# Kernel tuning notes

Hardware: AMD Instinct MI355X
Metric: run time of the kernel (lower is better)

The kernel has to match this reference:

```python
import jax, jax.numpy as jnp
import numpy as np
from jax import lax

NUM_GROUP = 512
GROUP_SIZE = 32


def fps(xyz, npoint):
    """Farthest point sampling. xyz: [B, N, 3] -> centers [B, npoint, 3]."""
    B, N, _ = xyz.shape
    big = jnp.asarray(1e10, xyz.dtype)

    def body(carry, _):
        min_d, farthest = carry  # [B, N], [B]
        centroid = jnp.take_along_axis(xyz, farthest[:, None, None], axis=1)  # [B,1,3]
        d = jnp.sum((xyz - centroid) ** 2, axis=-1)  # [B, N]
        min_d = jnp.minimum(min_d, d)
        nxt = jnp.argmax(min_d, axis=-1).astype(jnp.int32)
        return (min_d, nxt), farthest

    init = (jnp.full((B, N), big, xyz.dtype), jnp.zeros((B,), jnp.int32))
    _, idxs = lax.scan(body, init, None, length=npoint)  # [npoint, B]
    idxs = idxs.T  # [B, npoint]
    return jnp.take_along_axis(xyz, idxs[..., None], axis=1)  # [B, npoint, 3]


def knn_idx(xyz, center, k):
    """xyz [B,N,3], center [B,G,3] -> idx [B,G,k] of k nearest (squared L2)."""
    # [B, G, N] squared distances
    d2 = jnp.sum((center[:, :, None, :] - xyz[:, None, :, :]) ** 2, axis=-1)
    _, idx = lax.top_k(-d2, k)  # smallest distances
    return idx


def setup_inputs() -> dict:
    key = jax.random.key(0)
    xyz = jax.random.normal(key, (32, 3, 8192), dtype=jnp.float32)
    return {"xyz": xyz}


def reference(xyz):
    # xyz: [B, 3, N] -> [B, N, 3]
    pts = jnp.transpose(xyz, (0, 2, 1))[:, :, :3]
    B, N, _ = pts.shape
    center = fps(pts, NUM_GROUP)                  # [B, G, 3]
    idx = knn_idx(pts, center, GROUP_SIZE)        # [B, G, k]
    flat_idx = idx.reshape(B, NUM_GROUP * GROUP_SIZE)
    neighborhood = jnp.take_along_axis(pts, flat_idx[..., None], axis=1)
    neighborhood = neighborhood.reshape(B, NUM_GROUP, GROUP_SIZE, 3)
    neighborhood = neighborhood - center[:, :, None, :]
    return neighborhood, center
```

## Files before the change

### kernel.cpp

```cpp
#include <hip/hip_runtime.h>

typedef unsigned long long u64;
typedef unsigned int u32;
typedef float v2f __attribute__((ext_vector_type(2)));

#define BATCH 32
#define NPTS  8192
#define NGRP  512
#define KNN_K 32

#define FPS_T 256
#define FPS_W (FPS_T / 64)
#define PPAIR (NPTS / FPS_T / 2)

#define KNN_WPB 8
#define KNN_T   (KNN_WPB * 64)
#define QCAP    128

#define NCH     (NPTS / 64)
#define GC      16
#define NCELL   (GC * GC * GC)
#define QB      512
#define BT      512
#define BPT     (NPTS / BT)
#define WSF     (4 * NPTS + NCH * 6)

__device__ __forceinline__ float sq3(float dx, float dy, float dz) {
    return __fadd_rn(__fadd_rn(__fmul_rn(dx, dx), __fmul_rn(dy, dy)), __fmul_rn(dz, dz));
}

__device__ __forceinline__ u64 packdi(float d, int n) {
    return ((u64)__float_as_uint(d) << 32) | (u32)n;
}

__device__ __forceinline__ u64 umin64(u64 a, u64 b) { return a < b ? a : b; }
__device__ __forceinline__ u64 umax64(u64 a, u64 b) { return a > b ? a : b; }

__device__ __forceinline__ u64 shfl_xor_u64(u64 v, int m) {
    int lo = __shfl_xor((int)(u32)v, m, 64);
    int hi = __shfl_xor((int)(u32)(v >> 32), m, 64);
    return ((u64)(u32)hi << 32) | (u32)lo;
}

__device__ __forceinline__ u64 shfl_u64(u64 v, int src) {
    int lo = __shfl((int)(u32)v, src, 64);
    int hi = __shfl((int)(u32)(v >> 32), src, 64);
    return ((u64)(u32)hi << 32) | (u32)lo;
}

template <int CTRL>
__device__ __forceinline__ u64 dpp_max_step(u64 k) {
    u32 plo = (u32)__builtin_amdgcn_update_dpp(0, (int)(u32)k, CTRL, 0xF, 0xF, true);
    u32 phi = (u32)__builtin_amdgcn_update_dpp(0, (int)(u32)(k >> 32), CTRL, 0xF, 0xF, true);
    u64 p = ((u64)phi << 32) | plo;
    return k > p ? k : p;
}
__device__ __forceinline__ u64 dpp_wave_max(u64 k) {
    k = dpp_max_step<0x111>(k);
    k = dpp_max_step<0x112>(k);
    k = dpp_max_step<0x114>(k);
    k = dpp_max_step<0x118>(k);
    k = dpp_max_step<0x142>(k);
    k = dpp_max_step<0x143>(k);
    return k;
}

__device__ __forceinline__ u64 lane_sort64(u64 v, int lane) {
#pragma unroll
    for (int k = 2; k <= 64; k <<= 1) {
#pragma unroll
        for (int j = k >> 1; j > 0; j >>= 1) {
            u64 p = shfl_xor_u64(v, j);
            bool keepmin = (((lane & k) == 0) == ((lane & j) == 0));
            u64 mn = umin64(v, p), mx = umax64(v, p);
            v = keepmin ? mn : mx;
        }
    }
    return v;
}

__device__ __forceinline__ u64 lane_merge64(u64 m, u64 c, int lane) {
    u64 cr = shfl_xor_u64(c, 63);
    u64 z = umin64(m, cr);
#pragma unroll
    for (int dd = 32; dd > 0; dd >>= 1) {
        u64 p = shfl_xor_u64(z, dd);
        u64 mn = umin64(z, p), mx = umax64(z, p);
        z = (lane & dd) ? mx : mn;
    }
    return z;
}

__device__ __forceinline__ void knn_step(u64& m, u64& tau, int& cnt, u64* sbuf,
                                         float x, float y, float z,
                                         float cx, float cy, float cz,
                                         int n, int lane) {
    float d = sq3(__fsub_rn(x, cx), __fsub_rn(y, cy), __fsub_rn(z, cz));
    u64 kk = packdi(d, n);
    bool cand = kk < tau;
    u64 mask = __ballot(cand);
    if (mask) {
        u32 below = __builtin_amdgcn_mbcnt_hi(
            (u32)(mask >> 32), __builtin_amdgcn_mbcnt_lo((u32)mask, 0));
        if (cand) sbuf[cnt + below] = kk;
        cnt += (int)__popcll(mask);
        if (cnt >= 64) {
            u64 c = sbuf[lane];
            c = lane_sort64(c, lane);
            m = lane_merge64(m, c, lane);
            tau = shfl_u64(m, 31);
            int rem = cnt - 64;
            if (lane < rem) sbuf[lane] = sbuf[64 + lane];
            cnt = rem;
        }
    }
}

__global__ __launch_bounds__(FPS_T) void fps_kernel(const float* __restrict__ in,
                                                    float* __restrict__ centers) {
#pragma clang fp contract(off)
    __shared__ float sx[NPTS];
    __shared__ float sy[NPTS];
    __shared__ float sz[NPTS];
    __shared__ u64 s_key[2][FPS_W];
    __shared__ float s_out[NGRP * 3];

    const int b = blockIdx.x;
    const int t = threadIdx.x;
    const int w = t >> 6;
    const float* xp = in + (size_t)b * 3 * NPTS;
    const float* yp = xp + NPTS;
    const float* zp = xp + 2 * NPTS;

    v2f xr[PPAIR], yr[PPAIR], zr[PPAIR], md[PPAIR];
#pragma unroll
    for (int i = 0; i < PPAIR; ++i) {
        int n = i * (2 * FPS_T) + 2 * t;
        xr[i] = *(const v2f*)(xp + n);
        yr[i] = *(const v2f*)(yp + n);
        zr[i] = *(const v2f*)(zp + n);
        *(v2f*)(sx + n) = xr[i];
        *(v2f*)(sy + n) = yr[i];
        *(v2f*)(sz + n) = zr[i];
        md[i] = (v2f){1e10f, 1e10f};
    }
    __syncthreads();

    int cur = 0;
    for (int r = 0; r < NGRP; ++r) {
        const float cx = sx[cur], cy = sy[cur], cz = sz[cur];
        if (t == 0) {
            s_out[r * 3 + 0] = cx;
            s_out[r * 3 + 1] = cy;
            s_out[r * 3 + 2] = cz;
        }

        float bd0 = -1.0f, bd1 = -1.0f;
        int   bi0 = 0,     bi1 = 0;
#pragma unroll
        for (int i = 0; i < PPAIR; ++i) {
            v2f dx = xr[i] - cx;
            v2f dy = yr[i] - cy;
            v2f dz = zr[i] - cz;
            v2f dd = dx * dx + dy * dy + dz * dz;
            md[i] = __builtin_elementwise_min(md[i], dd);
            int n = i * (2 * FPS_T) + 2 * t;
            if (md[i].x > bd0) { bd0 = md[i].x; bi0 = n; }
            if (md[i].y > bd1) { bd1 = md[i].y; bi1 = n + 1; }
        }
        u64 k0 = ((u64)__float_as_uint(bd0) << 32) | (u32)(~(u32)bi0);
        u64 k1 = ((u64)__float_as_uint(bd1) << 32) | (u32)(~(u32)bi1);
        u64 k = dpp_wave_max(umax64(k0, k1));
        if ((t & 63) == 63) s_key[r & 1][w] = k;
        __syncthreads();
        u64 m = umax64(umax64(s_key[r & 1][0], s_key[r & 1][1]),
                       umax64(s_key[r & 1][2], s_key[r & 1][3]));
        cur = (int)(~(u32)m);
    }

    __syncthreads();
    float* cdst = centers + (size_t)b * NGRP * 3;
    for (int i = t; i < NGRP * 3; i += FPS_T) cdst[i] = s_out[i];
}

__device__ __forceinline__ int qbin(float v) {
    int c = (int)((v + 4.0f) * 64.0f);
    c = c < 0 ? 0 : c;
    return c > (QB - 1) ? (QB - 1) : c;
}
__device__ __forceinline__ u32 part3_4(u32 v) {
    return (v & 1u) | ((v & 2u) << 2) | ((v & 4u) << 4) | ((v & 8u) << 6);
}

__global__ __launch_bounds__(BT) void build_kernel(const float* __restrict__ in,
                                                   float* __restrict__ ws) {
    __shared__ u32 hist[NCELL];
    __shared__ u32 hq[3][QB];
    __shared__ float sxl[NPTS];
    __shared__ float syl[NPTS];
    __shared__ float szl[NPTS];
    __shared__ u32 wtot[3][BT / 64];

    const int b = blockIdx.x;
    const int t = threadIdx.x;
    const int lane = t & 63;
    const int w = t >> 6;
    const float* xp = in + (size_t)b * 3 * NPTS;
    const float* yp = xp + NPTS;
    const float* zp = xp + 2 * NPTS;
    float* wsb = ws + (size_t)b * WSF;
    float* ws_sx = wsb;
    float* ws_sy = wsb + NPTS;
    float* ws_sz = wsb + 2 * NPTS;
    u32*   ws_si = (u32*)(wsb + 3 * NPTS);
    float* ws_ab = wsb + 4 * NPTS;

    for (int i = t; i < NCELL; i += BT) hist[i] = 0;
    for (int i = t; i < 3 * QB; i += BT) (&hq[0][0])[i] = 0;
    __syncthreads();

    float px[BPT], py[BPT], pz[BPT];
#pragma unroll
    for (int i = 0; i < BPT; ++i) {
        int n = i * BT + t;
        px[i] = xp[n]; py[i] = yp[n]; pz[i] = zp[n];
        atomicAdd(&hq[0][qbin(px[i])], 1u);
        atomicAdd(&hq[1][qbin(py[i])], 1u);
        atomicAdd(&hq[2][qbin(pz[i])], 1u);
    }
    __syncthreads();

    {
        u32 v0 = hq[0][t], v1 = hq[1][t], v2 = hq[2][t];
        u32 x0 = v0, x1 = v1, x2 = v2;
#pragma unroll
        for (int d = 1; d < 64; d <<= 1) {
            u32 y0 = __shfl_up(x0, d, 64), y1 = __shfl_up(x1, d, 64), y2 = __shfl_up(x2, d, 64);
            if (lane >= d) { x0 += y0; x1 += y1; x2 += y2; }
        }
        if (lane == 63) { wtot[0][w] = x0; wtot[1][w] = x1; wtot[2][w] = x2; }
        __syncthreads();
        u32 b0 = 0, b1 = 0, b2 = 0;
        for (int j = 0; j < w; ++j) { b0 += wtot[0][j]; b1 += wtot[1][j]; b2 += wtot[2][j]; }
        hq[0][t] = (b0 + x0 - v0) >> 9;
        hq[1][t] = (b1 + x1 - v1) >> 9;
        hq[2][t] = (b2 + x2 - v2) >> 9;
    }
    __syncthreads();

    int pc[BPT];
#pragma unroll
    for (int i = 0; i < BPT; ++i) {
        u32 cxq = hq[0][qbin(px[i])];
        u32 cyq = hq[1][qbin(py[i])];
        u32 czq = hq[2][qbin(pz[i])];
        pc[i] = (int)(part3_4(cxq) | (part3_4(cyq) << 1) | (part3_4(czq) << 2));
        atomicAdd(&hist[pc[i]], 1u);
    }
    __syncthreads();

    u32 h[NCELL / BT];
    u32 lsum = 0;
#pragma unroll
    for (int j = 0; j < NCELL / BT; ++j) { h[j] = hist[t * (NCELL / BT) + j]; lsum += h[j]; }
    u32 x = lsum;
#pragma unroll
    for (int d = 1; d < 64; d <<= 1) {
        u32 y = __shfl_up(x, d, 64);
        if (lane >= d) x += y;
    }
    if (lane == 63) wtot[0][w] = x;
    u32 wexcl = x - lsum;
    __syncthreads();
    u32 base = 0;
    for (int j = 0; j < w; ++j) base += wtot[0][j];
    u32 run = base + wexcl;
#pragma unroll
    for (int j = 0; j < NCELL / BT; ++j) {
        u32 c = h[j];
        hist[t * (NCELL / BT) + j] = run;
        run += c;
    }
    __syncthreads();

#pragma unroll
    for (int i = 0; i < BPT; ++i) {
        u32 pos = atomicAdd(&hist[pc[i]], 1u);
        sxl[pos] = px[i]; syl[pos] = py[i]; szl[pos] = pz[i];
        ws_si[pos] = (u32)(i * BT + t);
    }
    __syncthreads();

    for (int i = t; i < NPTS; i += BT) {
        ws_sx[i] = sxl[i]; ws_sy[i] = syl[i]; ws_sz[i] = szl[i];
    }
    for (int q = w; q < NCH; q += BT / 64) {
        int p = q * 64 + lane;
        float X = sxl[p], Y = syl[p], Z = szl[p];
        float xlo = X, xhi = X, ylo = Y, yhi = Y, zlo = Z, zhi = Z;
#pragma unroll
        for (int d = 1; d < 64; d <<= 1) {
            xlo = fminf(xlo, __shfl_xor(xlo, d, 64)); xhi = fmaxf(xhi, __shfl_xor(xhi, d, 64));
            ylo = fminf(ylo, __shfl_xor(ylo, d, 64)); yhi = fmaxf(yhi, __shfl_xor(yhi, d, 64));
            zlo = fminf(zlo, __shfl_xor(zlo, d, 64)); zhi = fmaxf(zhi, __shfl_xor(zhi, d, 64));
        }
        if (lane == 0) {
            float* a = ws_ab + q * 6;
            a[0] = xlo; a[1] = xhi; a[2] = ylo; a[3] = yhi; a[4] = zlo; a[5] = zhi;
        }
    }
}

__global__ __launch_bounds__(KNN_T) void knn_kernel(const float* __restrict__ in,
                                                    const float* __restrict__ centers,
                                                    const float* __restrict__ ws,
                                                    float* __restrict__ out) {
    __shared__ float s_ab[NCH * 6];
    __shared__ u64 sbuf[KNN_WPB][QCAP];

    const int wave = threadIdx.x >> 6;
    const int lane = threadIdx.x & 63;
    const int cid  = blockIdx.x * KNN_WPB + wave;
    const int b    = cid >> 9;

    const float* xp = in + (size_t)b * 3 * NPTS;
    const float* yp = xp + NPTS;
    const float* zp = xp + 2 * NPTS;
    const float* wsb = ws + (size_t)b * WSF;
    const float* sxs = wsb;
    const float* sys = wsb + NPTS;
    const float* szs = wsb + 2 * NPTS;
    const u32*   sidx = (const u32*)(wsb + 3 * NPTS);
    const float* ab = wsb + 4 * NPTS;

    for (int i = threadIdx.x; i < NCH * 6; i += KNN_T) s_ab[i] = ab[i];
    __syncthreads();

    const float cx = centers[cid * 3 + 0];
    const float cy = centers[cid * 3 + 1];
    const float cz = centers[cid * 3 + 2];

    u64 k0, k1;
    {
        const float* a0 = &s_ab[lane * 6];
        float dx = fmaxf(fmaxf(__fsub_rn(a0[0], cx), __fsub_rn(cx, a0[1])), 0.0f);
        float dy = fmaxf(fmaxf(__fsub_rn(a0[2], cy), __fsub_rn(cy, a0[3])), 0.0f);
        float dz = fmaxf(fmaxf(__fsub_rn(a0[4], cz), __fsub_rn(cz, a0[5])), 0.0f);
        k0 = ((u64)__float_as_uint(dx * dx + dy * dy + dz * dz) << 32) | (u32)lane;
        const float* a1 = &s_ab[(lane + 64) * 6];
        dx = fmaxf(fmaxf(__fsub_rn(a1[0], cx), __fsub_rn(cx, a1[1])), 0.0f);
        dy = fmaxf(fmaxf(__fsub_rn(a1[2], cy), __fsub_rn(cy, a1[3])), 0.0f);
        dz = fmaxf(fmaxf(__fsub_rn(a1[4], cz), __fsub_rn(cz, a1[5])), 0.0f);
        k1 = ((u64)__float_as_uint(dx * dx + dy * dy + dz * dz) << 32) | (u32)(lane + 64);
    }

    u64 m, tau;
    int cnt = 0;

    {
        u64 inv = dpp_wave_max(~umin64(k0, k1));
        u64 got = ~shfl_u64(inv, 63);
        int c = (int)(u32)got;
        int p = c * 64 + lane;
        float X = sxs[p], Y = sys[p], Z = szs[p];
        int n = (int)sidx[p];
        m = lane_sort64(packdi(sq3(__fsub_rn(X, cx), __fsub_rn(Y, cy), __fsub_rn(Z, cz)), n),
                        lane);
        tau = shfl_u64(m, 31);
        if (lane == (c & 63)) { if (c < 64) k0 = ~0ull; else k1 = ~0ull; }
    }

    for (int it = 1; it < NCH; ++it) {
        u64 inv = dpp_wave_max(~umin64(k0, k1));
        u64 got = ~shfl_u64(inv, 63);
        float lb = __uint_as_float((u32)(got >> 32));
        float tau_d = __uint_as_float((u32)(tau >> 32));
        if (lb * 0.999f > tau_d) break;
        int c = (int)(u32)got;
        int p = c * 64 + lane;
        float X = sxs[p], Y = sys[p], Z = szs[p];
        int n = (int)sidx[p];
        knn_step(m, tau, cnt, sbuf[wave], X, Y, Z, cx, cy, cz, n, lane);
        if (lane == (c & 63)) { if (c < 64) k0 = ~0ull; else k1 = ~0ull; }
    }

    while (cnt > 0) {
        int take = cnt < 64 ? cnt : 64;
        u64 v = sbuf[wave][lane];
        u64 c = (lane < take) ? v : ~0ull;
        c = lane_sort64(c, lane);
        m = lane_merge64(m, c, lane);
        int rem = cnt - take;
        if (lane < rem) sbuf[wave][lane] = sbuf[wave][64 + lane];
        cnt = rem;
    }

    if (lane < KNN_K) {
        int n = (int)(u32)m;
        size_t o = (size_t)cid * (KNN_K * 3) + (size_t)lane * 3;
        out[o + 0] = __fsub_rn(xp[n], cx);
        out[o + 1] = __fsub_rn(yp[n], cy);
        out[o + 2] = __fsub_rn(zp[n], cz);
    }
}

#define KNN_WPB_FB 4
__global__ __launch_bounds__(KNN_WPB_FB * 64) void knn_fallback(
    const float* __restrict__ in, const float* __restrict__ centers,
    float* __restrict__ out) {
    __shared__ u64 sbuf[KNN_WPB_FB][QCAP];

    const int wave = threadIdx.x >> 6;
    const int lane = threadIdx.x & 63;
    const int cid  = blockIdx.x * KNN_WPB_FB + wave;
    const int b    = cid >> 9;

    const float* xp = in + (size_t)b * 3 * NPTS;
    const float* yp = xp + NPTS;
    const float* zp = xp + 2 * NPTS;

    const float cx = centers[cid * 3 + 0];
    const float cy = centers[cid * 3 + 1];
    const float cz = centers[cid * 3 + 2];

    float x = xp[lane], y = yp[lane], z = zp[lane];
    u64 m = packdi(sq3(__fsub_rn(x, cx), __fsub_rn(y, cy), __fsub_rn(z, cz)), lane);
    m = lane_sort64(m, lane);
    u64 tau = shfl_u64(m, 31);
    int cnt = 0;

    int j = 1;
#pragma unroll 1
    for (; j + 3 < NPTS / 64; j += 4) {
        int n0 = j * 64 + lane, n1 = n0 + 64, n2 = n0 + 128, n3 = n0 + 192;
        float x0 = xp[n0], y0 = yp[n0], z0 = zp[n0];
        float x1 = xp[n1], y1 = yp[n1], z1 = zp[n1];
        float x2 = xp[n2], y2 = yp[n2], z2 = zp[n2];
        float x3 = xp[n3], y3 = yp[n3], z3 = zp[n3];
        knn_step(m, tau, cnt, sbuf[wave], x0, y0, z0, cx, cy, cz, n0, lane);
        knn_step(m, tau, cnt, sbuf[wave], x1, y1, z1, cx, cy, cz, n1, lane);
        knn_step(m, tau, cnt, sbuf[wave], x2, y2, z2, cx, cy, cz, n2, lane);
        knn_step(m, tau, cnt, sbuf[wave], x3, y3, z3, cx, cy, cz, n3, lane);
    }
    for (; j < NPTS / 64; ++j) {
        int n = j * 64 + lane;
        knn_step(m, tau, cnt, sbuf[wave], xp[n], yp[n], zp[n], cx, cy, cz, n, lane);
    }
    while (cnt > 0) {
        int take = cnt < 64 ? cnt : 64;
        u64 v = sbuf[wave][lane];
        u64 c = (lane < take) ? v : ~0ull;
        c = lane_sort64(c, lane);
        m = lane_merge64(m, c, lane);
        int rem = cnt - take;
        if (lane < rem) sbuf[wave][lane] = sbuf[wave][64 + lane];
        cnt = rem;
    }
    if (lane < KNN_K) {
        int n = (int)(u32)m;
        size_t o = (size_t)cid * (KNN_K * 3) + (size_t)lane * 3;
        out[o + 0] = __fsub_rn(xp[n], cx);
        out[o + 1] = __fsub_rn(yp[n], cy);
        out[o + 2] = __fsub_rn(zp[n], cz);
    }
}

extern "C" void kernel_launch(void* const* d_in, const int* in_sizes, int n_in,
                              void* d_out, int out_size, void* d_ws, size_t ws_size,
                              hipStream_t stream) {
    const float* in  = (const float*)d_in[0];
    float* out       = (float*)d_out;
    float* centers   = out + (size_t)BATCH * NGRP * KNN_K * 3;

    const size_t need = (size_t)BATCH * WSF * sizeof(float);

    fps_kernel<<<BATCH, FPS_T, 0, stream>>>(in, centers);
    if (d_ws != nullptr && ws_size >= need) {
        build_kernel<<<BATCH, BT, 0, stream>>>(in, (float*)d_ws);
        knn_kernel<<<(BATCH * NGRP) / KNN_WPB, KNN_T, 0, stream>>>(
            in, centers, (const float*)d_ws, out);
    } else {
        knn_fallback<<<(BATCH * NGRP) / KNN_WPB_FB, KNN_WPB_FB * 64, 0, stream>>>(
            in, centers, out);
    }
}
```

Before: 555.5 us.

## Fuse FPS and grid-build kernels into one launch with block-range dispatch

Merges the farthest-point-sampling kernel and the spatial grid build kernel into a single launch of 2*BATCH blocks. The first BATCH blocks run FPS and the rest build the cell-sorted point workspace, so the short build work runs concurrently with the serial FPS instead of after it. The build path drops to 256 threads and re-reads the inputs from global memory rather than holding them in registers. The shared LDS is sized to the larger layout via a union-like byte buffer, which may reduce occupancy for the FPS blocks.

```diff
diff --git a/kernel.cpp b/kernel.cpp
--- a/kernel.cpp
+++ b/kernel.cpp
@@ -21,8 +21,7 @@
 #define GC      16
 #define NCELL   (GC * GC * GC)
 #define QB      512
-#define BT      512
-#define BPT     (NPTS / BT)
+#define CBT     256
 #define WSF     (4 * NPTS + NCH * 6)
 
 __device__ __forceinline__ float sq3(float dx, float dy, float dz) {
@@ -116,73 +115,6 @@
     }
 }
 
-__global__ __launch_bounds__(FPS_T) void fps_kernel(const float* __restrict__ in,
-                                                    float* __restrict__ centers) {
-#pragma clang fp contract(off)
-    __shared__ float sx[NPTS];
-    __shared__ float sy[NPTS];
-    __shared__ float sz[NPTS];
-    __shared__ u64 s_key[2][FPS_W];
-    __shared__ float s_out[NGRP * 3];
-
-    const int b = blockIdx.x;
-    const int t = threadIdx.x;
-    const int w = t >> 6;
-    const float* xp = in + (size_t)b * 3 * NPTS;
-    const float* yp = xp + NPTS;
-    const float* zp = xp + 2 * NPTS;
-
-    v2f xr[PPAIR], yr[PPAIR], zr[PPAIR], md[PPAIR];
-#pragma unroll
-    for (int i = 0; i < PPAIR; ++i) {
-        int n = i * (2 * FPS_T) + 2 * t;
-        xr[i] = *(const v2f*)(xp + n);
-        yr[i] = *(const v2f*)(yp + n);
-        zr[i] = *(const v2f*)(zp + n);
-        *(v2f*)(sx + n) = xr[i];
-        *(v2f*)(sy + n) = yr[i];
-        *(v2f*)(sz + n) = zr[i];
-        md[i] = (v2f){1e10f, 1e10f};
-    }
-    __syncthreads();
-
-    int cur = 0;
-    for (int r = 0; r < NGRP; ++r) {
-        const float cx = sx[cur], cy = sy[cur], cz = sz[cur];
-        if (t == 0) {
-            s_out[r * 3 + 0] = cx;
-            s_out[r * 3 + 1] = cy;
-            s_out[r * 3 + 2] = cz;
-        }
-
-        float bd0 = -1.0f, bd1 = -1.0f;
-        int   bi0 = 0,     bi1 = 0;
-#pragma unroll
-        for (int i = 0; i < PPAIR; ++i) {
-            v2f dx = xr[i] - cx;
-            v2f dy = yr[i] - cy;
-            v2f dz = zr[i] - cz;
-            v2f dd = dx * dx + dy * dy + dz * dz;
-            md[i] = __builtin_elementwise_min(md[i], dd);
-            int n = i * (2 * FPS_T) + 2 * t;
-            if (md[i].x > bd0) { bd0 = md[i].x; bi0 = n; }
-            if (md[i].y > bd1) { bd1 = md[i].y; bi1 = n + 1; }
-        }
-        u64 k0 = ((u64)__float_as_uint(bd0) << 32) | (u32)(~(u32)bi0);
-        u64 k1 = ((u64)__float_as_uint(bd1) << 32) | (u32)(~(u32)bi1);
-        u64 k = dpp_wave_max(umax64(k0, k1));
-        if ((t & 63) == 63) s_key[r & 1][w] = k;
-        __syncthreads();
-        u64 m = umax64(umax64(s_key[r & 1][0], s_key[r & 1][1]),
-                       umax64(s_key[r & 1][2], s_key[r & 1][3]));
-        cur = (int)(~(u32)m);
-    }
-
-    __syncthreads();
-    float* cdst = centers + (size_t)b * NGRP * 3;
-    for (int i = t; i < NGRP * 3; i += FPS_T) cdst[i] = s_out[i];
-}
-
 __device__ __forceinline__ int qbin(float v) {
     int c = (int)((v + 4.0f) * 64.0f);
     c = c < 0 ? 0 : c;
@@ -192,19 +124,89 @@
     return (v & 1u) | ((v & 2u) << 2) | ((v & 4u) << 4) | ((v & 8u) << 6);
 }
 
-__global__ __launch_bounds__(BT) void build_kernel(const float* __restrict__ in,
-                                                   float* __restrict__ ws) {
-    __shared__ u32 hist[NCELL];
-    __shared__ u32 hq[3][QB];
-    __shared__ float sxl[NPTS];
-    __shared__ float syl[NPTS];
-    __shared__ float szl[NPTS];
-    __shared__ u32 wtot[3][BT / 64];
-
-    const int b = blockIdx.x;
+struct FpsLds {
+    float sx[NPTS]; float sy[NPTS]; float sz[NPTS];
+    u64 s_key[2][FPS_W];
+    float s_out[NGRP * 3];
+};
+struct BldLds {
+    u32 hist[NCELL];
+    u32 hq[3][QB];
+    float sxl[NPTS]; float syl[NPTS]; float szl[NPTS];
+    u32 wtot[3][CBT / 64];
+};
+
+__global__ __launch_bounds__(CBT) void fps_build_kernel(const float* __restrict__ in,
+                                                        float* __restrict__ ws,
+                                                        float* __restrict__ centers) {
+#pragma clang fp contract(off)
+    __shared__ alignas(16) char smem[sizeof(BldLds)];
+
     const int t = threadIdx.x;
     const int lane = t & 63;
     const int w = t >> 6;
+
+    if (blockIdx.x < BATCH) {
+        FpsLds& S = *reinterpret_cast<FpsLds*>(smem);
+        const int b = blockIdx.x;
+        const float* xp = in + (size_t)b * 3 * NPTS;
+        const float* yp = xp + NPTS;
+        const float* zp = xp + 2 * NPTS;
+
+        v2f xr[PPAIR], yr[PPAIR], zr[PPAIR], md[PPAIR];
+#pragma unroll
+        for (int i = 0; i < PPAIR; ++i) {
+            int n = i * (2 * FPS_T) + 2 * t;
+            xr[i] = *(const v2f*)(xp + n);
+            yr[i] = *(const v2f*)(yp + n);
+            zr[i] = *(const v2f*)(zp + n);
+            *(v2f*)(S.sx + n) = xr[i];
+            *(v2f*)(S.sy + n) = yr[i];
+            *(v2f*)(S.sz + n) = zr[i];
+            md[i] = (v2f){1e10f, 1e10f};
+        }
+        __syncthreads();
+
+        int cur = 0;
+        for (int r = 0; r < NGRP; ++r) {
+            const float cx = S.sx[cur], cy = S.sy[cur], cz = S.sz[cur];
+            if (t == 0) {
+                S.s_out[r * 3 + 0] = cx;
+                S.s_out[r * 3 + 1] = cy;
+                S.s_out[r * 3 + 2] = cz;
+            }
+
+            float bd0 = -1.0f, bd1 = -1.0f;
+            int   bi0 = 0,     bi1 = 0;
+#pragma unroll
+            for (int i = 0; i < PPAIR; ++i) {
+                v2f dx = xr[i] - cx;
+                v2f dy = yr[i] - cy;
+                v2f dz = zr[i] - cz;
+                v2f dd = dx * dx + dy * dy + dz * dz;
+                md[i] = __builtin_elementwise_min(md[i], dd);
+                int n = i * (2 * FPS_T) + 2 * t;
+                if (md[i].x > bd0) { bd0 = md[i].x; bi0 = n; }
+                if (md[i].y > bd1) { bd1 = md[i].y; bi1 = n + 1; }
+            }
+            u64 k0 = ((u64)__float_as_uint(bd0) << 32) | (u32)(~(u32)bi0);
+            u64 k1 = ((u64)__float_as_uint(bd1) << 32) | (u32)(~(u32)bi1);
+            u64 k = dpp_wave_max(umax64(k0, k1));
+            if ((t & 63) == 63) S.s_key[r & 1][w] = k;
+            __syncthreads();
+            u64 m = umax64(umax64(S.s_key[r & 1][0], S.s_key[r & 1][1]),
+                           umax64(S.s_key[r & 1][2], S.s_key[r & 1][3]));
+            cur = (int)(~(u32)m);
+        }
+
+        __syncthreads();
+        float* cdst = centers + (size_t)b * NGRP * 3;
+        for (int i = t; i < NGRP * 3; i += FPS_T) cdst[i] = S.s_out[i];
+        return;
+    }
+
+    BldLds& S = *reinterpret_cast<BldLds*>(smem);
+    const int b = blockIdx.x - BATCH;
     const float* xp = in + (size_t)b * 3 * NPTS;
     const float* yp = xp + NPTS;
     const float* zp = xp + 2 * NPTS;
@@ -215,88 +217,89 @@
     u32*   ws_si = (u32*)(wsb + 3 * NPTS);
     float* ws_ab = wsb + 4 * NPTS;
 
-    for (int i = t; i < NCELL; i += BT) hist[i] = 0;
-    for (int i = t; i < 3 * QB; i += BT) (&hq[0][0])[i] = 0;
-    __syncthreads();
-
-    float px[BPT], py[BPT], pz[BPT];
-#pragma unroll
-    for (int i = 0; i < BPT; ++i) {
-        int n = i * BT + t;
-        px[i] = xp[n]; py[i] = yp[n]; pz[i] = zp[n];
-        atomicAdd(&hq[0][qbin(px[i])], 1u);
-        atomicAdd(&hq[1][qbin(py[i])], 1u);
-        atomicAdd(&hq[2][qbin(pz[i])], 1u);
+    for (int i = t; i < NCELL; i += CBT) S.hist[i] = 0;
+    for (int i = t; i < 3 * QB; i += CBT) (&S.hq[0][0])[i] = 0;
+    __syncthreads();
+
+    for (int i = t; i < NPTS; i += CBT) {
+        atomicAdd(&S.hq[0][qbin(xp[i])], 1u);
+        atomicAdd(&S.hq[1][qbin(yp[i])], 1u);
+        atomicAdd(&S.hq[2][qbin(zp[i])], 1u);
     }
     __syncthreads();
 
     {
-        u32 v0 = hq[0][t], v1 = hq[1][t], v2 = hq[2][t];
-        u32 x0 = v0, x1 = v1, x2 = v2;
+        u32 va0 = S.hq[0][2 * t], vb0 = S.hq[0][2 * t + 1];
+        u32 va1 = S.hq[1][2 * t], vb1 = S.hq[1][2 * t + 1];
+        u32 va2 = S.hq[2][2 * t], vb2 = S.hq[2][2 * t + 1];
+        u32 s0 = va0 + vb0, s1 = va1 + vb1, s2 = va2 + vb2;
+        u32 x0 = s0, x1 = s1, x2 = s2;
 #pragma unroll
         for (int d = 1; d < 64; d <<= 1) {
             u32 y0 = __shfl_up(x0, d, 64), y1 = __shfl_up(x1, d, 64), y2 = __shfl_up(x2, d, 64);
             if (lane >= d) { x0 += y0; x1 += y1; x2 += y2; }
         }
-        if (lane == 63) { wtot[0][w] = x0; wtot[1][w] = x1; wtot[2][w] = x2; }
+        if (lane == 63) { S.wtot[0][w] = x0; S.wtot[1][w] = x1; S.wtot[2][w] = x2; }
         __syncthreads();
         u32 b0 = 0, b1 = 0, b2 = 0;
-        for (int j = 0; j < w; ++j) { b0 += wtot[0][j]; b1 += wtot[1][j]; b2 += wtot[2][j]; }
-        hq[0][t] = (b0 + x0 - v0) >> 9;
-        hq[1][t] = (b1 + x1 - v1) >> 9;
-        hq[2][t] = (b2 + x2 - v2) >> 9;
-    }
-    __syncthreads();
-
-    int pc[BPT];
-#pragma unroll
-    for (int i = 0; i < BPT; ++i) {
-        u32 cxq = hq[0][qbin(px[i])];
-        u32 cyq = hq[1][qbin(py[i])];
-        u32 czq = hq[2][qbin(pz[i])];
-        pc[i] = (int)(part3_4(cxq) | (part3_4(cyq) << 1) | (part3_4(czq) << 2));
-        atomicAdd(&hist[pc[i]], 1u);
-    }
-    __syncthreads();
-
-    u32 h[NCELL / BT];
-    u32 lsum = 0;
-#pragma unroll
-    for (int j = 0; j < NCELL / BT; ++j) { h[j] = hist[t * (NCELL / BT) + j]; lsum += h[j]; }
-    u32 x = lsum;
-#pragma unroll
-    for (int d = 1; d < 64; d <<= 1) {
-        u32 y = __shfl_up(x, d, 64);
-        if (lane >= d) x += y;
-    }
-    if (lane == 63) wtot[0][w] = x;
-    u32 wexcl = x - lsum;
-    __syncthreads();
-    u32 base = 0;
-    for (int j = 0; j < w; ++j) base += wtot[0][j];
-    u32 run = base + wexcl;
-#pragma unroll
-    for (int j = 0; j < NCELL / BT; ++j) {
-        u32 c = h[j];
-        hist[t * (NCELL / BT) + j] = run;
-        run += c;
-    }
-    __syncthreads();
-
-#pragma unroll
-    for (int i = 0; i < BPT; ++i) {
-        u32 pos = atomicAdd(&hist[pc[i]], 1u);
-        sxl[pos] = px[i]; syl[pos] = py[i]; szl[pos] = pz[i];
-        ws_si[pos] = (u32)(i * BT + t);
-    }
-    __syncthreads();
-
-    for (int i = t; i < NPTS; i += BT) {
-        ws_sx[i] = sxl[i]; ws_sy[i] = syl[i]; ws_sz[i] = szl[i];
-    }
-    for (int q = w; q < NCH; q += BT / 64) {
+        for (int j = 0; j < w; ++j) { b0 += S.wtot[0][j]; b1 += S.wtot[1][j]; b2 += S.wtot[2][j]; }
+        u32 e0 = b0 + x0 - s0, e1 = b1 + x1 - s1, e2 = b2 + x2 - s2;
+        S.hq[0][2 * t] = e0 >> 9;  S.hq[0][2 * t + 1] = (e0 + va0) >> 9;
+        S.hq[1][2 * t] = e1 >> 9;  S.hq[1][2 * t + 1] = (e1 + va1) >> 9;
+        S.hq[2][2 * t] = e2 >> 9;  S.hq[2][2 * t + 1] = (e2 + va2) >> 9;
+    }
+    __syncthreads();
+
+    for (int i = t; i < NPTS; i += CBT) {
+        int pc = (int)(part3_4(S.hq[0][qbin(xp[i])]) |
+                       (part3_4(S.hq[1][qbin(yp[i])]) << 1) |
+                       (part3_4(S.hq[2][qbin(zp[i])]) << 2));
+        atomicAdd(&S.hist[pc], 1u);
+    }
+    __syncthreads();
+
+    {
+        u32 h[NCELL / CBT];
+        u32 lsum = 0;
+#pragma unroll
+        for (int j = 0; j < NCELL / CBT; ++j) { h[j] = S.hist[t * (NCELL / CBT) + j]; lsum += h[j]; }
+        u32 x = lsum;
+#pragma unroll
+        for (int d = 1; d < 64; d <<= 1) {
+            u32 y = __shfl_up(x, d, 64);
+            if (lane >= d) x += y;
+        }
+        if (lane == 63) S.wtot[0][w] = x;
+        __syncthreads();
+        u32 base = 0;
+        for (int j = 0; j < w; ++j) base += S.wtot[0][j];
+        u32 run = base + x - lsum;
+#pragma unroll
+        for (int j = 0; j < NCELL / CBT; ++j) {
+            u32 c = h[j];
+            S.hist[t * (NCELL / CBT) + j] = run;
+            run += c;
+        }
+    }
+    __syncthreads();
+
+    for (int i = t; i < NPTS; i += CBT) {
+        float X = xp[i], Y = yp[i], Z = zp[i];
+        int pc = (int)(part3_4(S.hq[0][qbin(X)]) |
+                       (part3_4(S.hq[1][qbin(Y)]) << 1) |
+                       (part3_4(S.hq[2][qbin(Z)]) << 2));
+        u32 pos = atomicAdd(&S.hist[pc], 1u);
+        S.sxl[pos] = X; S.syl[pos] = Y; S.szl[pos] = Z;
+        ws_si[pos] = (u32)i;
+    }
+    __syncthreads();
+
+    for (int i = t; i < NPTS; i += CBT) {
+        ws_sx[i] = S.sxl[i]; ws_sy[i] = S.syl[i]; ws_sz[i] = S.szl[i];
+    }
+    for (int q = w; q < NCH; q += CBT / 64) {
         int p = q * 64 + lane;
-        float X = sxl[p], Y = syl[p], Z = szl[p];
+        float X = S.sxl[p], Y = S.syl[p], Z = S.szl[p];
         float xlo = X, xhi = X, ylo = Y, yhi = Y, zlo = Z, zhi = Z;
 #pragma unroll
         for (int d = 1; d < 64; d <<= 1) {
@@ -404,6 +407,72 @@
     }
 }
 
+__global__ __launch_bounds__(FPS_T) void fps_kernel(const float* __restrict__ in,
+                                                    float* __restrict__ centers) {
+#pragma clang fp contract(off)
+    __shared__ float sx[NPTS];
+    __shared__ float sy[NPTS];
+    __shared__ float sz[NPTS];
+    __shared__ u64 s_key[2][FPS_W];
+    __shared__ float s_out[NGRP * 3];
+
+    const int b = blockIdx.x;
+    const int t = threadIdx.x;
+    const int w = t >> 6;
+    const float* xp = in + (size_t)b * 3 * NPTS;
+    const float* yp = xp + NPTS;
+    const float* zp = xp + 2 * NPTS;
+
+    v2f xr[PPAIR], yr[PPAIR], zr[PPAIR], md[PPAIR];
+#pragma unroll
+    for (int i = 0; i < PPAIR; ++i) {
+        int n = i * (2 * FPS_T) + 2 * t;
+        xr[i] = *(const v2f*)(xp + n);
+        yr[i] = *(const v2f*)(yp + n);
+        zr[i] = *(const v2f*)(zp + n);
+        *(v2f*)(sx + n) = xr[i];
+        *(v2f*)(sy + n) = yr[i];
+        *(v2f*)(sz + n) = zr[i];
+        md[i] = (v2f){1e10f, 1e10f};
+    }
+    __syncthreads();
+
+    int cur = 0;
+    for (int r = 0; r < NGRP; ++r) {
+        const float cx = sx[cur], cy = sy[cur], cz = sz[cur];
+        if (t == 0) {
+            s_out[r * 3 + 0] = cx;
+            s_out[r * 3 + 1] = cy;
+            s_out[r * 3 + 2] = cz;
+        }
+        float bd0 = -1.0f, bd1 = -1.0f;
+        int   bi0 = 0,     bi1 = 0;
+#pragma unroll
+        for (int i = 0; i < PPAIR; ++i) {
+            v2f dx = xr[i] - cx;
+            v2f dy = yr[i] - cy;
+            v2f dz = zr[i] - cz;
+            v2f dd = dx * dx + dy * dy + dz * dz;
+            md[i] = __builtin_elementwise_min(md[i], dd);
+            int n = i * (2 * FPS_T) + 2 * t;
+            if (md[i].x > bd0) { bd0 = md[i].x; bi0 = n; }
+            if (md[i].y > bd1) { bd1 = md[i].y; bi1 = n + 1; }
+        }
+        u64 k0 = ((u64)__float_as_uint(bd0) << 32) | (u32)(~(u32)bi0);
+        u64 k1 = ((u64)__float_as_uint(bd1) << 32) | (u32)(~(u32)bi1);
+        u64 k = dpp_wave_max(umax64(k0, k1));
+        if ((t & 63) == 63) s_key[r & 1][w] = k;
+        __syncthreads();
+        u64 m = umax64(umax64(s_key[r & 1][0], s_key[r & 1][1]),
+                       umax64(s_key[r & 1][2], s_key[r & 1][3]));
+        cur = (int)(~(u32)m);
+    }
+
+    __syncthreads();
+    float* cdst = centers + (size_t)b * NGRP * 3;
+    for (int i = t; i < NGRP * 3; i += FPS_T) cdst[i] = s_out[i];
+}
+
 #define KNN_WPB_FB 4
 __global__ __launch_bounds__(KNN_WPB_FB * 64) void knn_fallback(
     const float* __restrict__ in, const float* __restrict__ centers,
@@ -474,12 +543,12 @@
 
     const size_t need = (size_t)BATCH * WSF * sizeof(float);
 
-    fps_kernel<<<BATCH, FPS_T, 0, stream>>>(in, centers);
     if (d_ws != nullptr && ws_size >= need) {
-        build_kernel<<<BATCH, BT, 0, stream>>>(in, (float*)d_ws);
+        fps_build_kernel<<<2 * BATCH, CBT, 0, stream>>>(in, (float*)d_ws, centers);
         knn_kernel<<<(BATCH * NGRP) / KNN_WPB, KNN_T, 0, stream>>>(
             in, centers, (const float*)d_ws, out);
     } else {
+        fps_kernel<<<BATCH, FPS_T, 0, stream>>>(in, centers);
         knn_fallback<<<(BATCH * NGRP) / KNN_WPB_FB, KNN_WPB_FB * 64, 0, stream>>>(
             in, centers, out);
     }
```

Measured after the change: 530.9 us, median of 3. 1.05x faster.
